# Performance work log

Hardware: AMD Instinct MI355X
Metric: run time of the kernel (lower is better)

## Reference

```python
import jax, jax.numpy as jnp
import numpy as np

B = 8192
NOISE = 25


def setup_inputs() -> dict:
    key = jax.random.key(0)
    ks = jax.random.split(key, 16)
    rn = lambda k, s: jax.random.normal(k, s, dtype=jnp.float32)
    return {
        "z": rn(ks[0], (B, 3)),
        "z_next": rn(ks[1], (B, 3)),
        "n": rn(ks[2], (B, NOISE)),
        "prior": rn(ks[3], (B, 4611)),
        "w1_W": rn(ks[4], (NOISE, 192)) * 0.2, "w1_b": rn(ks[5], (192,)) * 0.1,
        "b1_W": rn(ks[6], (NOISE, 64)) * 0.2, "b1_b": rn(ks[7], (64,)) * 0.1,
        "w2_W": rn(ks[8], (NOISE, 4096)) * 0.2, "w2_b": rn(ks[9], (4096,)) * 0.1,
        "b2_W": rn(ks[10], (NOISE, 64)) * 0.2, "b2_b": rn(ks[11], (64,)) * 0.1,
        "w3_W": rn(ks[12], (NOISE, 192)) * 0.2, "w3_b": rn(ks[13], (192,)) * 0.1,
        "b3_W": rn(ks[14], (NOISE, 3)) * 0.2, "b3_b": rn(ks[15], (3,)) * 0.1,
    }


def _pairwise_dist(A, Bm):
    # sqrt(sum_d (A_i - B_j)^2 + 1e-8) computed via the norm identity -> one GEMM
    sq = (jnp.sum(A * A, axis=1)[:, None]
          + jnp.sum(Bm * Bm, axis=1)[None, :]
          - 2.0 * (A @ Bm.T))
    return jnp.sqrt(jnp.maximum(sq, 0.0) + 1e-8)


def reference(z, z_next, n, prior,
              w1_W, w1_b, b1_W, b1_b,
              w2_W, w2_b, b2_W, b2_b,
              w3_W, w3_b, b3_W, b3_b):
    bs = z.shape[0]
    # hypernetwork: per-sample decoder weights from noise n (B, 25)
    W1 = (n @ w1_W + w1_b).reshape(bs, 64, 3)
    B1 = n @ b1_W + b1_b                       # (B, 64)
    W2 = (n @ w2_W + w2_b).reshape(bs, 64, 64)
    B2 = n @ b2_W + b2_b                       # (B, 64)
    W3 = (n @ w3_W + w3_b).reshape(bs, 3, 64)
    B3 = n @ b3_W + b3_b                       # (B, 3)
    # decode: per-sample bmm chain with ELU
    h = jax.nn.elu(jnp.einsum('bij,bj->bi', W1, z) + B1)
    h = jax.nn.elu(jnp.einsum('bij,bj->bi', W2, h) + B2)
    z_hat = jnp.einsum('bij,bj->bi', W3, h) + B3
    recon = jnp.mean(jnp.sum((z_hat - z_next) ** 2, axis=1))
    # KL estimator over flattened generated weights, D = 4611
    G = jnp.concatenate([W1.reshape(bs, -1), B1, W2.reshape(bs, -1), B2,
                         W3.reshape(bs, -1), B3], axis=1)
    wp = jnp.min(_pairwise_dist(prior, G), axis=0)   # nearest prior sample per gen sample
    idx = jnp.arange(bs)
    ww_mat = _pairwise_dist(G, G).at[idx, idx].add(1e10)
    ww = jnp.min(ww_mat, axis=0)
    D = G.shape[1]
    kl = jnp.mean(jnp.log(wp / (ww + 1e-8) + 1e-8)) * D
    kl = kl + jnp.log(jnp.float32(bs) / jnp.float32(bs - 1))
    return recon, kl, z_hat
```

## Files before the change

### kernel.cpp

```cpp
#include <hip/hip_runtime.h>
#include <math.h>

#define BATCH 8192
#define D_G   4611
#define DGP   4624
#define KN    25
#define KE    28

#define WS_WCAT   0
#define WS_BCAT   115600
#define WS_WCATT  120224
#define WS_M      249344
#define WS_C      249984
#define WS_BB     250016
#define WS_PPAD   250048
#define WS_Q      479424
#define WS_G2     487616
#define WS_RPAD   495808
#define WS_WP2    725184
#define WS_WW2    733376
#define WS_ACC    741568
#define WS_H1T    741600
#define WS_H2T    1265888

__device__ inline float eluf(float x) { return x > 0.f ? x : expm1f(x); }

__device__ inline float sdot26(const float* __restrict__ WT, int rowidx, const float* nx) {
  const float* row = WT + (size_t)__builtin_amdgcn_readfirstlane(rowidx) * KE;
  float acc = row[25];
#pragma unroll
  for (int k = 0; k < 25; k++) acc = fmaf(row[k], nx[k], acc);
  return acc;
}

__global__ void k_init(float* ws) {
  int idx = blockIdx.x * 256 + threadIdx.x;
  unsigned int* u = (unsigned int*)ws;
  if (idx < BATCH)            u[WS_WP2 + idx] = 0x7F7FFFFFu;
  else if (idx < 2 * BATCH)   u[WS_WW2 + (idx - BATCH)] = 0x7F7FFFFFu;
  else if (idx == 2 * BATCH)  ws[WS_ACC] = 0.f;
}

__global__ void k_build(const float* __restrict__ w1W, const float* __restrict__ w1b,
                        const float* __restrict__ b1W, const float* __restrict__ b1b,
                        const float* __restrict__ w2W, const float* __restrict__ w2b,
                        const float* __restrict__ b2W, const float* __restrict__ b2b,
                        const float* __restrict__ w3W, const float* __restrict__ w3b,
                        const float* __restrict__ b3W, const float* __restrict__ b3b,
                        float* ws) {
  int idx = blockIdx.x * 256 + threadIdx.x;
  if (idx >= KN * D_G) return;
  int k = idx / D_G;
  int d = idx - k * D_G;
  float wv, bv;
  if (d < 192)       { int c = d;        wv = w1W[k*192  + c]; bv = w1b[c]; }
  else if (d < 256)  { int c = d - 192;  wv = b1W[k*64   + c]; bv = b1b[c]; }
  else if (d < 4352) { int c = d - 256;  wv = w2W[k*4096 + c]; bv = w2b[c]; }
  else if (d < 4416) { int c = d - 4352; wv = b2W[k*64   + c]; bv = b2b[c]; }
  else if (d < 4608) { int c = d - 4416; wv = w3W[k*192  + c]; bv = w3b[c]; }
  else               { int c = d - 4608; wv = b3W[k*3    + c]; bv = b3b[c]; }
  ws[WS_WCAT  + k * DGP + d] = wv;
  ws[WS_WCATT + d * KE  + k] = wv;
  if (k == 0) {
    ws[WS_BCAT + d] = bv;
    ws[WS_WCATT + d * KE + 25] = bv;
    ws[WS_WCATT + d * KE + 26] = 0.f;
    ws[WS_WCATT + d * KE + 27] = 0.f;
  }
}

__global__ __launch_bounds__(256) void k_M(float* ws) {
  const float* Wc = ws + WS_WCAT;
  const float* bc = ws + WS_BCAT;
  __shared__ float part[4][26];
  int a = blockIdx.x, t = threadIdx.x;
  int wv = t >> 6, l = t & 63;
  if (a < 25) {
    float acc[26];
#pragma unroll
    for (int v = 0; v < 26; v++) acc[v] = 0.f;
    for (int d = t; d < D_G; d += 256) {
      float va = Wc[a * DGP + d];
#pragma unroll
      for (int b = 0; b < 25; b++) acc[b] += va * Wc[b * DGP + d];
      acc[25] += va * bc[d];
    }
#pragma unroll
    for (int v = 0; v < 26; v++) {
      float x = acc[v];
#pragma unroll
      for (int off = 32; off > 0; off >>= 1) x += __shfl_down(x, off, 64);
      if (l == 0) part[wv][v] = x;
    }
    __syncthreads();
    if (t < 26) {
      float s = part[0][t] + part[1][t] + part[2][t] + part[3][t];
      if (t < 25) ws[WS_M + a * 25 + t] = s; else ws[WS_C + a] = s;
    }
  } else {
    float acc = 0.f;
    for (int d = t; d < D_G; d += 256) { float b = bc[d]; acc += b * b; }
#pragma unroll
    for (int off = 32; off > 0; off >>= 1) acc += __shfl_down(acc, off, 64);
    if (l == 0) part[wv][0] = acc;
    __syncthreads();
    if (t == 0) ws[WS_BB] = part[0][0] + part[1][0] + part[2][0] + part[3][0];
  }
}

__global__ void k_persample(const float* __restrict__ n, float* ws) {
  int j = blockIdx.x * 256 + threadIdx.x;
  if (j >= BATCH) return;
  const float* M  = ws + WS_M;
  const float* cv = ws + WS_C;
  float nr[25];
#pragma unroll
  for (int k = 0; k < 25; k++) nr[k] = n[j * 25 + k];
  float q = 0.f;
  for (int k2 = 0; k2 < 25; k2++) {
    float p = 0.f;
#pragma unroll
    for (int k1 = 0; k1 < 25; k1++) p += nr[k1] * M[k1 * 25 + k2];
    ws[WS_PPAD + j * KE + k2] = p;
    q += p * nr[k2];
  }
  float nc = 0.f;
#pragma unroll
  for (int k = 0; k < 25; k++) nc += nr[k] * cv[k];
  ws[WS_PPAD + j * KE + 25] = -0.5f * q;
  ws[WS_PPAD + j * KE + 26] = 0.f;
  ws[WS_PPAD + j * KE + 27] = 0.f;
  ws[WS_Q  + j] = q;
  ws[WS_G2 + j] = q + 2.f * nc + ws[WS_BB];
}

__global__ __launch_bounds__(256) void k_prior(const float* __restrict__ prior, float* ws) {
  const float* wc = ws + WS_WCAT;
  const float* bc = ws + WS_BCAT;
  int t = threadIdx.x;
  int wv = t >> 6, l = t & 63;
  int i0 = (blockIdx.x * 4 + wv) * 2;
  const float* pr0 = prior + (size_t)i0 * D_G;

  float racc[2][25];
  float sacc[2], p2acc[2];
#pragma unroll
  for (int r = 0; r < 2; r++) {
    sacc[r] = 0.f; p2acc[r] = 0.f;
#pragma unroll
    for (int k = 0; k < 25; k++) racc[r][k] = 0.f;
  }

  for (int ch = 0; ch < 18; ++ch) {
    int base = ch * 256 + 4 * l;
    float pv0[4], pv1[4];
#pragma unroll
    for (int q = 0; q < 4; q++) pv0[q] = pr0[base + q];
#pragma unroll
    for (int q = 0; q < 4; q++) pv1[q] = pr0[(size_t)D_G + base + q];
    float4 bl = *(const float4*)(wc + (size_t)25 * DGP + base);
    p2acc[0] += pv0[0]*pv0[0] + pv0[1]*pv0[1] + pv0[2]*pv0[2] + pv0[3]*pv0[3];
    sacc[0]  += pv0[0]*bl.x + pv0[1]*bl.y + pv0[2]*bl.z + pv0[3]*bl.w;
    p2acc[1] += pv1[0]*pv1[0] + pv1[1]*pv1[1] + pv1[2]*pv1[2] + pv1[3]*pv1[3];
    sacc[1]  += pv1[0]*bl.x + pv1[1]*bl.y + pv1[2]*bl.z + pv1[3]*bl.w;
#pragma unroll
    for (int k = 0; k < 25; k++) {
      float4 w = *(const float4*)(wc + (size_t)k * DGP + base);
      racc[0][k] += pv0[0]*w.x + pv0[1]*w.y + pv0[2]*w.z + pv0[3]*w.w;
      racc[1][k] += pv1[0]*w.x + pv1[1]*w.y + pv1[2]*w.z + pv1[3]*w.w;
    }
  }

  if (l < 3) {
    int d = 4608 + l;
#pragma unroll
    for (int r = 0; r < 2; r++) {
      float pvt = pr0[(size_t)r * D_G + d];
      p2acc[r] += pvt * pvt;
      sacc[r]  += pvt * bc[d];
#pragma unroll
      for (int k = 0; k < 25; k++) racc[r][k] += pvt * wc[(size_t)k * DGP + d];
    }
  }
#pragma unroll
  for (int r = 0; r < 2; r++) {
#pragma unroll
    for (int k = 0; k < 25; k++) {
      float v = racc[r][k];
#pragma unroll
      for (int off = 32; off > 0; off >>= 1) v += __shfl_down(v, off, 64);
      if (l == 0) ws[WS_RPAD + (size_t)(i0 + r) * KE + k] = v;
    }
    float s = sacc[r], p2 = p2acc[r];
#pragma unroll
    for (int off = 32; off > 0; off >>= 1) { s += __shfl_down(s, off, 64); p2 += __shfl_down(p2, off, 64); }
    if (l == 0) {
      ws[WS_RPAD + (size_t)(i0 + r) * KE + 25] = -0.5f * (p2 - 2.f * s);
      ws[WS_RPAD + (size_t)(i0 + r) * KE + 26] = 0.f;
      ws[WS_RPAD + (size_t)(i0 + r) * KE + 27] = 0.f;
    }
  }
}

template <int SKIP>
__global__ __launch_bounds__(256) void k_pair(const float* __restrict__ APAD,
                                              const float* __restrict__ Bn,
                                              const float* __restrict__ beta,
                                              unsigned int* __restrict__ outm) {
  __shared__ float rows[256 * KE];
  int t = threadIdx.x;
  int jbase = blockIdx.y * 256;
  {
    const float4* src = (const float4*)(APAD + (size_t)jbase * KE);
    float4* dst = (float4*)rows;
#pragma unroll
    for (int u = 0; u < 7; u++) dst[t + 256 * u] = src[t + 256 * u];
  }
  int j0 = blockIdx.x * 512 + t;
  int j1 = j0 + 256;
  float nx0[25], nx1[25];
#pragma unroll
  for (int k = 0; k < 25; k++) { nx0[k] = Bn[j0 * 25 + k]; nx1[k] = Bn[j1 * 25 + k]; }
  float bj0 = beta[j0], bj1 = beta[j1];
  float mn0 = 3.402823466e38f, mn1 = 3.402823466e38f;
  __syncthreads();
#pragma unroll 2
  for (int it = 0; it < 256; ++it) {
    const float* row = rows + it * KE;
    float a0 = row[25], a1 = row[25];
#pragma unroll
    for (int k = 0; k < 25; k++) { a0 = fmaf(row[k], nx0[k], a0); a1 = fmaf(row[k], nx1[k], a1); }
    float sq0 = fmaxf(fmaf(-2.f, a0, bj0), 0.f);
    float sq1 = fmaxf(fmaf(-2.f, a1, bj1), 0.f);
    int i = jbase + it;
    bool sk0 = SKIP && (i == j0);
    bool sk1 = SKIP && (i == j1);
    mn0 = sk0 ? mn0 : fminf(mn0, sq0);
    mn1 = sk1 ? mn1 : fminf(mn1, sq1);
  }
  atomicMin(&outm[j0], __float_as_uint(mn0));
  atomicMin(&outm[j1], __float_as_uint(mn1));
}

__global__ __launch_bounds__(64) void kd1(const float* __restrict__ n, const float* __restrict__ z,
                                          const float* __restrict__ ws_wt, float* __restrict__ h1t) {
  int s = blockIdx.x * 64 + threadIdx.x;
  int rb = blockIdx.y * 16;
  float nx[25];
#pragma unroll
  for (int k = 0; k < 25; k++) nx[k] = n[s * 25 + k];
  float zr[3];
#pragma unroll
  for (int d = 0; d < 3; d++) zr[d] = z[s * 3 + d];
  for (int r = 0; r < 16; r++) {
    int rr = rb + r;
    float acc = sdot26(ws_wt, 192 + rr, nx);
#pragma unroll
    for (int d = 0; d < 3; d++)
      acc = fmaf(sdot26(ws_wt, rr * 3 + d, nx), zr[d], acc);
    h1t[rr * BATCH + s] = eluf(acc);
  }
}

__global__ __launch_bounds__(64) void kd2(const float* __restrict__ n,
                                          const float* __restrict__ ws_wt,
                                          const float* __restrict__ h1t, float* __restrict__ h2t) {
  int s = blockIdx.x * 64 + threadIdx.x;
  int rb = blockIdx.y * 4;
  float nx[25];
#pragma unroll
  for (int k = 0; k < 25; k++) nx[k] = n[s * 25 + k];
  float acc[4];
#pragma unroll
  for (int r = 0; r < 4; r++) acc[r] = sdot26(ws_wt, 4352 + rb + r, nx);
  for (int c = 0; c < 64; c++) {
    float h1c = h1t[c * BATCH + s];
#pragma unroll
    for (int r = 0; r < 4; r++) {
      float w = sdot26(ws_wt, 256 + (rb + r) * 64 + c, nx);
      acc[r] = fmaf(w, h1c, acc[r]);
    }
  }
#pragma unroll
  for (int r = 0; r < 4; r++) h2t[(rb + r) * BATCH + s] = eluf(acc[r]);
}

__global__ __launch_bounds__(64) void kd3(const float* __restrict__ n,
                                          const float* __restrict__ znext,
                                          const float* __restrict__ ws_wt,
                                          const float* __restrict__ h2t,
                                          float* __restrict__ out, float* __restrict__ accum) {
  int s = blockIdx.x * 64 + threadIdx.x;
  int r = blockIdx.y;
  float nx[25];
#pragma unroll
  for (int k = 0; k < 25; k++) nx[k] = n[s * 25 + k];
  float acc = sdot26(ws_wt, 4608 + r, nx);
  for (int c = 0; c < 64; c++)
    acc = fmaf(sdot26(ws_wt, 4416 + r * 64 + c, nx), h2t[c * BATCH + s], acc);
  out[2 + s * 3 + r] = acc;
  float dz = acc - znext[s * 3 + r];
  float v = dz * dz;
#pragma unroll
  for (int off = 32; off > 0; off >>= 1) v += __shfl_down(v, off, 64);
  if (threadIdx.x == 0) atomicAdd(accum, v);
}

__global__ void k_finish(float* ws, float* __restrict__ out) {
  __shared__ float sred[256];
  int t = threadIdx.x;
  float part = 0.f;
  for (int j = t; j < BATCH; j += 256) {
    float wp2 = ws[WS_WP2 + j];
    float ww2 = ws[WS_WW2 + j];
    float wp = sqrtf(wp2 + 1e-8f);
    float ww = sqrtf(ww2 + 1e-8f);
    part += logf(wp / (ww + 1e-8f) + 1e-8f);
  }
  sred[t] = part; __syncthreads();
  for (int off = 128; off > 0; off >>= 1) { if (t < off) sred[t] += sred[t + off]; __syncthreads(); }
  if (t == 0) {
    float kl = sred[0] / (float)BATCH * (float)D_G + logf((float)BATCH / (float)(BATCH - 1));
    out[0] = ws[WS_ACC] / (float)BATCH;
    out[1] = kl;
  }
}

extern "C" void kernel_launch(void* const* d_in, const int* in_sizes, int n_in,
                              void* d_out, int out_size, void* d_ws, size_t ws_size,
                              hipStream_t stream) {
  (void)in_sizes; (void)n_in; (void)out_size; (void)ws_size;
  const float* z     = (const float*)d_in[0];
  const float* znext = (const float*)d_in[1];
  const float* n     = (const float*)d_in[2];
  const float* prior = (const float*)d_in[3];
  const float* w1W = (const float*)d_in[4];  const float* w1b = (const float*)d_in[5];
  const float* b1W = (const float*)d_in[6];  const float* b1b = (const float*)d_in[7];
  const float* w2W = (const float*)d_in[8];  const float* w2b = (const float*)d_in[9];
  const float* b2W = (const float*)d_in[10]; const float* b2b = (const float*)d_in[11];
  const float* w3W = (const float*)d_in[12]; const float* w3b = (const float*)d_in[13];
  const float* b3W = (const float*)d_in[14]; const float* b3b = (const float*)d_in[15];
  float* out = (float*)d_out;
  float* ws  = (float*)d_ws;

  k_init<<<dim3(65), dim3(256), 0, stream>>>(ws);
  k_build<<<dim3((KN * D_G + 255) / 256), dim3(256), 0, stream>>>(
      w1W, w1b, b1W, b1b, w2W, w2b, b2W, b2b, w3W, w3b, b3W, b3b, ws);
  k_M<<<dim3(26), dim3(256), 0, stream>>>(ws);
  k_persample<<<dim3(32), dim3(256), 0, stream>>>(n, ws);
  k_prior<<<dim3(1024), dim3(256), 0, stream>>>(prior, ws);
  k_pair<1><<<dim3(16, 32), dim3(256), 0, stream>>>(ws + WS_PPAD, n, ws + WS_Q,
                                                    (unsigned int*)(ws + WS_WW2));
  k_pair<0><<<dim3(16, 32), dim3(256), 0, stream>>>(ws + WS_RPAD, n, ws + WS_G2,
                                                    (unsigned int*)(ws + WS_WP2));
  kd1<<<dim3(128, 4), dim3(64), 0, stream>>>(n, z, ws + WS_WCATT, ws + WS_H1T);
  kd2<<<dim3(128, 16), dim3(64), 0, stream>>>(n, ws + WS_WCATT, ws + WS_H1T, ws + WS_H2T);
  kd3<<<dim3(128, 3), dim3(64), 0, stream>>>(n, znext, ws + WS_WCATT, ws + WS_H2T, out, ws + WS_ACC);
  k_finish<<<dim3(1), dim3(256), 0, stream>>>(ws, out);
}
```

Measured before the change: 627.9 us.

## Pipeline prior projection with async global-to-LDS triple buffering and 4 rows per wave

The prior projection kernel now stages the shared weight chunks into LDS with asynchronous global_load_lds in a three-buffer pipeline, using manual vmcnt waits and barriers. Each wave now handles four prior rows instead of two, and the grid is halved so every weight tile is reused across more rows. The pair kernel also loads each LDS row as float4 vectors. This aims to cut redundant global weight traffic and hide load latency, but it raises register pressure (100 accumulators plus staged values) and depends on hand-tuned waitcnt counts.

Result: slower. 1.265 ms (+101.5%).

```diff
diff --git a/kernel.cpp b/kernel.cpp
--- a/kernel.cpp
+++ b/kernel.cpp
@@ -24,6 +24,11 @@
 #define WS_H2T    1265888
 
 __device__ inline float eluf(float x) { return x > 0.f ? x : expm1f(x); }
+
+__device__ __forceinline__ void gload_lds16(const float* g, float* l) {
+  __builtin_amdgcn_global_load_lds((const __attribute__((address_space(1))) unsigned int*)g,
+                                   (__attribute__((address_space(3))) unsigned int*)l, 16, 0, 0);
+}
 
 __device__ inline float sdot26(const float* __restrict__ WT, int rowidx, const float* nx) {
   const float* row = WT + (size_t)__builtin_amdgcn_readfirstlane(rowidx) * KE;
@@ -134,47 +139,99 @@
   ws[WS_G2 + j] = q + 2.f * nc + ws[WS_BB];
 }
 
-__global__ __launch_bounds__(256) void k_prior(const float* __restrict__ prior, float* ws) {
+__global__ __launch_bounds__(256, 2) void k_prior(const float* __restrict__ prior, float* ws) {
+  __shared__ float wlds[3][26 * 256];
   const float* wc = ws + WS_WCAT;
   const float* bc = ws + WS_BCAT;
   int t = threadIdx.x;
   int wv = t >> 6, l = t & 63;
-  int i0 = (blockIdx.x * 4 + wv) * 2;
+  int i0 = (blockIdx.x * 4 + wv) * 4;
   const float* pr0 = prior + (size_t)i0 * D_G;
 
-  float racc[2][25];
-  float sacc[2], p2acc[2];
-#pragma unroll
-  for (int r = 0; r < 2; r++) {
+  float racc[4][25];
+  float sacc[4], p2acc[4];
+#pragma unroll
+  for (int r = 0; r < 4; r++) {
     sacc[r] = 0.f; p2acc[r] = 0.f;
 #pragma unroll
     for (int k = 0; k < 25; k++) racc[r][k] = 0.f;
   }
 
-  for (int ch = 0; ch < 18; ++ch) {
-    int base = ch * 256 + 4 * l;
-    float pv0[4], pv1[4];
-#pragma unroll
-    for (int q = 0; q < 4; q++) pv0[q] = pr0[base + q];
-#pragma unroll
-    for (int q = 0; q < 4; q++) pv1[q] = pr0[(size_t)D_G + base + q];
-    float4 bl = *(const float4*)(wc + (size_t)25 * DGP + base);
-    p2acc[0] += pv0[0]*pv0[0] + pv0[1]*pv0[1] + pv0[2]*pv0[2] + pv0[3]*pv0[3];
-    sacc[0]  += pv0[0]*bl.x + pv0[1]*bl.y + pv0[2]*bl.z + pv0[3]*bl.w;
-    p2acc[1] += pv1[0]*pv1[0] + pv1[1]*pv1[1] + pv1[2]*pv1[2] + pv1[3]*pv1[3];
-    sacc[1]  += pv1[0]*bl.x + pv1[1]*bl.y + pv1[2]*bl.z + pv1[3]*bl.w;
-#pragma unroll
-    for (int k = 0; k < 25; k++) {
-      float4 w = *(const float4*)(wc + (size_t)k * DGP + base);
-      racc[0][k] += pv0[0]*w.x + pv0[1]*w.y + pv0[2]*w.z + pv0[3]*w.w;
-      racc[1][k] += pv1[0]*w.x + pv1[1]*w.y + pv1[2]*w.z + pv1[3]*w.w;
-    }
-  }
+  float pv0[4][4], pv1[4][4], pv2[4][4];
+
+#define PR_STAGE(BUF, CH) do {                                                   \
+    _Pragma("unroll")                                                            \
+    for (int u = 0; u < 7; u++) {                                                \
+      int row = u * 4 + wv;                                                      \
+      if (row >= 26) row = wv + 22;         \
+      gload_lds16(wc + (size_t)row * DGP + (CH) * 256 + 4 * l,                   \
+                  &wlds[BUF][row * 256]);                                        \
+    }                                                                            \
+  } while (0)
+
+#define PR_LOADPV(PV, CH) do {                                                   \
+    _Pragma("unroll")                                                            \
+    for (int r = 0; r < 4; r++)                                                  \
+      _Pragma("unroll")                                                          \
+      for (int q = 0; q < 4; q++)                                                \
+        PV[r][q] = pr0[(size_t)r * D_G + (CH) * 256 + 4 * l + q];                \
+  } while (0)
+
+#define PR_COMPUTE(BUF, PV) do {                                                 \
+    const float* wb = wlds[BUF];                                                 \
+    float4 bl = *(const float4*)&wb[25 * 256 + 4 * l];                           \
+    _Pragma("unroll")                                                            \
+    for (int r = 0; r < 4; r++) {                                                \
+      p2acc[r] += PV[r][0]*PV[r][0] + PV[r][1]*PV[r][1]                          \
+                + PV[r][2]*PV[r][2] + PV[r][3]*PV[r][3];                         \
+      sacc[r]  += PV[r][0]*bl.x + PV[r][1]*bl.y + PV[r][2]*bl.z + PV[r][3]*bl.w; \
+    }                                                                            \
+    _Pragma("unroll")                                                            \
+    for (int k = 0; k < 25; k++) {                                               \
+      float4 w = *(const float4*)&wb[k * 256 + 4 * l];                           \
+      _Pragma("unroll")                                                          \
+      for (int r = 0; r < 4; r++)                                                \
+        racc[r][k] += PV[r][0]*w.x + PV[r][1]*w.y + PV[r][2]*w.z + PV[r][3]*w.w; \
+    }                                                                            \
+  } while (0)
+
+  PR_STAGE(0, 0); PR_LOADPV(pv0, 0);
+  PR_STAGE(1, 1); PR_LOADPV(pv1, 1);
+
+  for (int tt = 0; tt < 5; ++tt) {
+    int c = 3 * tt;
+    __builtin_amdgcn_s_barrier();
+    PR_STAGE(2, c + 2); PR_LOADPV(pv2, c + 2);
+    asm volatile("s_waitcnt vmcnt(26)" ::: "memory");
+    PR_COMPUTE(0, pv0);
+    __builtin_amdgcn_s_barrier();
+    PR_STAGE(0, c + 3); PR_LOADPV(pv0, c + 3);
+    asm volatile("s_waitcnt vmcnt(26)" ::: "memory");
+    PR_COMPUTE(1, pv1);
+    __builtin_amdgcn_s_barrier();
+    PR_STAGE(1, c + 4); PR_LOADPV(pv1, c + 4);
+    asm volatile("s_waitcnt vmcnt(26)" ::: "memory");
+    PR_COMPUTE(2, pv2);
+  }
+  __builtin_amdgcn_s_barrier();
+  PR_STAGE(2, 17); PR_LOADPV(pv2, 17);
+  asm volatile("s_waitcnt vmcnt(26)" ::: "memory");
+  PR_COMPUTE(0, pv0);
+  __builtin_amdgcn_s_barrier();
+  asm volatile("s_waitcnt vmcnt(15)" ::: "memory");
+  PR_COMPUTE(1, pv1);
+  __builtin_amdgcn_s_barrier();
+  asm volatile("s_waitcnt vmcnt(4)" ::: "memory");
+  PR_COMPUTE(2, pv2);
+
+#undef PR_STAGE
+#undef PR_LOADPV
+#undef PR_COMPUTE
 
   if (l < 3) {
     int d = 4608 + l;
 #pragma unroll
-    for (int r = 0; r < 2; r++) {
+    for (int r = 0; r < 4; r++) {
       float pvt = pr0[(size_t)r * D_G + d];
       p2acc[r] += pvt * pvt;
       sacc[r]  += pvt * bc[d];
@@ -183,7 +240,7 @@
     }
   }
 #pragma unroll
-  for (int r = 0; r < 2; r++) {
+  for (int r = 0; r < 4; r++) {
 #pragma unroll
     for (int k = 0; k < 25; k++) {
       float v = racc[r][k];
@@ -207,7 +264,7 @@
                                               const float* __restrict__ Bn,
                                               const float* __restrict__ beta,
                                               unsigned int* __restrict__ outm) {
-  __shared__ float rows[256 * KE];
+  __shared__ float rows[256 * KE] __attribute__((aligned(16)));
   int t = threadIdx.x;
   int jbase = blockIdx.y * 256;
   {
@@ -226,10 +283,13 @@
   __syncthreads();
 #pragma unroll 2
   for (int it = 0; it < 256; ++it) {
-    const float* row = rows + it * KE;
-    float a0 = row[25], a1 = row[25];
-#pragma unroll
-    for (int k = 0; k < 25; k++) { a0 = fmaf(row[k], nx0[k], a0); a1 = fmaf(row[k], nx1[k], a1); }
+    const float4* rv = (const float4*)(rows + it * KE);
+    float rw[28];
+#pragma unroll
+    for (int u = 0; u < 7; u++) *(float4*)&rw[4 * u] = rv[u];
+    float a0 = rw[25], a1 = rw[25];
+#pragma unroll
+    for (int k = 0; k < 25; k++) { a0 = fmaf(rw[k], nx0[k], a0); a1 = fmaf(rw[k], nx1[k], a1); }
     float sq0 = fmaxf(fmaf(-2.f, a0, bj0), 0.f);
     float sq1 = fmaxf(fmaf(-2.f, a1, bj1), 0.f);
     int i = jbase + it;
@@ -348,7 +408,7 @@
       w1W, w1b, b1W, b1b, w2W, w2b, b2W, b2b, w3W, w3b, b3W, b3b, ws);
   k_M<<<dim3(26), dim3(256), 0, stream>>>(ws);
   k_persample<<<dim3(32), dim3(256), 0, stream>>>(n, ws);
-  k_prior<<<dim3(1024), dim3(256), 0, stream>>>(prior, ws);
+  k_prior<<<dim3(512), dim3(256), 0, stream>>>(prior, ws);
   k_pair<1><<<dim3(16, 32), dim3(256), 0, stream>>>(ws + WS_PPAD, n, ws + WS_Q,
                                                     (unsigned int*)(ws + WS_WW2));
   k_pair<0><<<dim3(16, 32), dim3(256), 0, stream>>>(ws + WS_RPAD, n, ws + WS_G2,
```
